# Optimization experiments

Measured on AMD Instinct MI355X. Metric: run time of the kernel, lower is better.

The kernel has to match this reference:

```python
import jax, jax.numpy as jnp
import numpy as np

N_NODES = 100000
N_EDGES = 1600000
F_IN = 128
F_HID = 16


def _gcn_conv(x, src, dst, W, b, n):
    # PyG GCNConv: x' = D^{-1/2} (A + I) D^{-1/2} (x W) + b
    h = x @ W                                   # [N, F_out] transform first (small F)
    deg = jax.ops.segment_sum(jnp.ones_like(dst, dtype=h.dtype), dst, num_segments=n)
    dinv = jnp.where(deg > 0, jax.lax.rsqrt(deg), 0.0)
    norm = dinv[src] * dinv[dst]                # [E+N] edge weights
    msg = h[src] * norm[:, None]                # gather + scale
    out = jax.ops.segment_sum(msg, dst, num_segments=n)  # scatter-add
    return out + b


def setup_inputs() -> dict:
    key = jax.random.key(0)
    k1, k2, k3, k4 = jax.random.split(key, 4)
    x = jax.random.normal(k1, (N_NODES, F_IN), dtype=jnp.float32)
    edge_index = jax.random.randint(k2, (2, N_EDGES), 0, N_NODES, dtype=jnp.int64)
    # Glorot-ish init for the two GCNConv weights
    W1 = jax.random.normal(k3, (F_IN, F_HID), dtype=jnp.float32) * (1.0 / np.sqrt(F_IN))
    b1 = jnp.zeros((F_HID,), dtype=jnp.float32)
    W2 = jax.random.normal(k4, (F_HID, F_IN), dtype=jnp.float32) * (1.0 / np.sqrt(F_HID))
    b2 = jnp.zeros((F_IN,), dtype=jnp.float32)
    return {"x": x, "edge_index": edge_index, "W1": W1, "b1": b1, "W2": W2, "b2": b2}


def reference(x, edge_index, W1, b1, W2, b2):
    n = x.shape[0]
    # add self-loops once (GCNConv default add_self_loops=True)
    loop = jnp.arange(n, dtype=edge_index.dtype)
    src = jnp.concatenate([edge_index[0], loop])
    dst = jnp.concatenate([edge_index[1], loop])
    h = _gcn_conv(x, src, dst, W1, b1, n)
    h = jax.nn.relu(h)
    out = _gcn_conv(h, src, dst, W2, b2, n)
    return out
```

## Files before the change

### kernel.cpp

```cpp
#include <hip/hip_runtime.h>
#include <hip/hip_fp16.h>


#define NN 100000
#define NE 1600000
#define FI 128
#define FH 16
#define CB 64
#define NB 1563
#define GC 512
#define CHUNK 3125
#define SCB 16

__device__ __forceinline__ float fc(const float4& v, int i) {
    return i == 0 ? v.x : i == 1 ? v.y : i == 2 ? v.z : v.w;
}

__global__ __launch_bounds__(256) void k_count(const int* __restrict__ dst,
                                               int* __restrict__ hist) {
    __shared__ int h[NB];
    for (int i = threadIdx.x; i < NB; i += 256) h[i] = 0;
    __syncthreads();
    int base = blockIdx.x * CHUNK;
    for (int i = base + threadIdx.x; i < base + CHUNK; i += 256)
        atomicAdd(&h[dst[i] >> 6], 1);
    __syncthreads();
    for (int b = threadIdx.x; b < NB; b += 256)
        hist[blockIdx.x * NB + b] = h[b];
}

__global__ __launch_bounds__(256) void k_scan_chunks(int* __restrict__ hist,
                                                     int* __restrict__ totals) {
    __shared__ int s[GC * SCB];
    int b0 = blockIdx.x * SCB;
    int o[GC * SCB / 256];
    #pragma unroll
    for (int r = 0; r < GC * SCB / 256; ++r) {
        int idx = r * 256 + threadIdx.x;
        int c = idx >> 4, bl = idx & (SCB - 1), b = b0 + bl;
        int v = (b < NB) ? hist[c * NB + b] : 0;
        s[idx] = v;
        o[r] = v;
    }
    __syncthreads();
    for (int off = 1; off < GC; off <<= 1) {
        int t[GC * SCB / 256];
        #pragma unroll
        for (int r = 0; r < GC * SCB / 256; ++r) {
            int idx = r * 256 + threadIdx.x;
            int c = idx >> 4;
            t[r] = (c >= off) ? s[idx - off * SCB] : 0;
        }
        __syncthreads();
        #pragma unroll
        for (int r = 0; r < GC * SCB / 256; ++r) {
            int idx = r * 256 + threadIdx.x;
            s[idx] += t[r];
        }
        __syncthreads();
    }
    #pragma unroll
    for (int r = 0; r < GC * SCB / 256; ++r) {
        int idx = r * 256 + threadIdx.x;
        int c = idx >> 4, bl = idx & (SCB - 1), b = b0 + bl;
        if (b < NB) {
            hist[c * NB + b] = s[idx] - o[r];
            if (c == GC - 1) totals[b] = s[idx];
        }
    }
}

__global__ __launch_bounds__(1024) void k_scan_buckets(const int* __restrict__ totals,
                                                       int* __restrict__ bucketStart,
                                                       int* __restrict__ rowStart) {
    __shared__ int s[1024];
    int tid = threadIdx.x;
    int i0 = 2 * tid, i1 = i0 + 1;
    int a = (i0 < NB) ? totals[i0] : 0;
    int b = (i1 < NB) ? totals[i1] : 0;
    s[tid] = a + b;
    __syncthreads();
    #pragma unroll
    for (int off = 1; off < 1024; off <<= 1) {
        int t = (tid >= off) ? s[tid - off] : 0;
        __syncthreads();
        s[tid] += t;
        __syncthreads();
    }
    int excl = s[tid] - (a + b);
    if (i0 < NB) bucketStart[i0] = excl;
    if (i1 < NB) bucketStart[i1] = excl + a;
    if (tid == 0) { bucketStart[NB] = NE; rowStart[NN] = NE; }
}

__global__ __launch_bounds__(256) void k_scatter(const int* __restrict__ src,
                                                 const int* __restrict__ dst,
                                                 const int* __restrict__ hist,
                                                 const int* __restrict__ bucketStart,
                                                 int* __restrict__ packed) {
    __shared__ int cur[NB];
    for (int b = threadIdx.x; b < NB; b += 256)
        cur[b] = hist[blockIdx.x * NB + b] + bucketStart[b];
    __syncthreads();
    int base = blockIdx.x * CHUNK;
    for (int i = base + threadIdx.x; i < base + CHUNK; i += 256) {
        int d = dst[i];
        int pos = atomicAdd(&cur[d >> 6], 1);
        packed[pos] = src[i] | ((d & 63) << 17);
    }
}

__global__ __launch_bounds__(256) void k_bsort(const int* __restrict__ packed,
                                               const int* __restrict__ bucketStart,
                                               int* __restrict__ csr,
                                               int* __restrict__ rowStart,
                                               float* __restrict__ dinv) {
    __shared__ int cnt[CB];
    __shared__ int rs[CB];
    __shared__ int cur[CB];
    if (threadIdx.x < CB) cnt[threadIdx.x] = 0;
    __syncthreads();
    int s0 = bucketStart[blockIdx.x], s1 = bucketStart[blockIdx.x + 1];
    for (int i = s0 + threadIdx.x; i < s1; i += 256)
        atomicAdd(&cnt[(packed[i] >> 17) & 63], 1);
    __syncthreads();
    if (threadIdx.x < CB) rs[threadIdx.x] = cnt[threadIdx.x];
    __syncthreads();
    #pragma unroll
    for (int off = 1; off < CB; off <<= 1) {
        int t = 0;
        if (threadIdx.x < CB && threadIdx.x >= off) t = rs[threadIdx.x - off];
        __syncthreads();
        if (threadIdx.x < CB) rs[threadIdx.x] += t;
        __syncthreads();
    }
    if (threadIdx.x < CB) {
        int start = s0 + rs[threadIdx.x] - cnt[threadIdx.x];
        cur[threadIdx.x] = start;
        int node = blockIdx.x * CB + threadIdx.x;
        if (node < NN) {
            rowStart[node] = start;
            dinv[node] = rsqrtf((float)(cnt[threadIdx.x] + 1));
        }
    }
    __syncthreads();
    for (int i = s0 + threadIdx.x; i < s1; i += 256) {
        int pk = packed[i];
        int pos = atomicAdd(&cur[(pk >> 17) & 63], 1);
        csr[pos] = pk & 131071;
    }
}

__global__ __launch_bounds__(256) void k_gemm1(const float* __restrict__ x,
                                               const float* __restrict__ W1,
                                               const float* __restrict__ dinv,
                                               __half2* __restrict__ g1) {
    __shared__ __align__(16) float w[FI * FH];
    float4* w4s = (float4*)w;
    w4s[threadIdx.x] = ((const float4*)W1)[threadIdx.x];
    w4s[threadIdx.x + 256] = ((const float4*)W1)[threadIdx.x + 256];
    __syncthreads();
    int fg = threadIdx.x & 3;
    int ng = threadIdx.x >> 2;
    int r0 = blockIdx.x * 256 + ng * 4;
    const float4* x4 = (const float4*)x;
    int rr[4]; bool val[4];
    #pragma unroll
    for (int i = 0; i < 4; ++i) {
        val[i] = (r0 + i < NN);
        rr[i] = val[i] ? r0 + i : NN - 1;
    }
    float acc[4][4];
    #pragma unroll
    for (int i = 0; i < 4; ++i)
        #pragma unroll
        for (int j = 0; j < 4; ++j) acc[i][j] = 0.f;
    #pragma unroll 2
    for (int k4 = 0; k4 < 32; ++k4) {
        float4 xv[4];
        #pragma unroll
        for (int i = 0; i < 4; ++i) xv[i] = x4[rr[i] * 32 + k4];
        #pragma unroll
        for (int kk = 0; kk < 4; ++kk) {
            float4 wv = w4s[(k4 * 4 + kk) * 4 + fg];
            #pragma unroll
            for (int i = 0; i < 4; ++i) {
                float xk = fc(xv[i], kk);
                acc[i][0] += xk * wv.x; acc[i][1] += xk * wv.y;
                acc[i][2] += xk * wv.z; acc[i][3] += xk * wv.w;
            }
        }
    }
    #pragma unroll
    for (int i = 0; i < 4; ++i) if (val[i]) {
        float dv = dinv[rr[i]];
        g1[rr[i] * 8 + fg * 2]     = __floats2half2_rn(acc[i][0] * dv, acc[i][1] * dv);
        g1[rr[i] * 8 + fg * 2 + 1] = __floats2half2_rn(acc[i][2] * dv, acc[i][3] * dv);
    }
}

template<bool RELU>
__global__ __launch_bounds__(256) void k_agg(const int* __restrict__ csr,
                                             const int* __restrict__ rowStart,
                                             const __half2* __restrict__ gin,
                                             const float* __restrict__ dinv,
                                             const float* __restrict__ b1,
                                             __half2* __restrict__ gh_out,
                                             float2* __restrict__ p2f) {
    int gid = blockIdx.x * 256 + threadIdx.x;
    int node = gid >> 3, c = gid & 7;
    if (node >= NN) return;
    int s0 = rowStart[node], s1 = rowStart[node + 1];
    float2 acc = __half22float2(gin[node * 8 + c]);
    int e = s0;
    for (; e + 3 < s1; e += 4) {
        int i0 = csr[e], i1 = csr[e + 1], i2 = csr[e + 2], i3 = csr[e + 3];
        float2 f0 = __half22float2(gin[i0 * 8 + c]);
        float2 f1 = __half22float2(gin[i1 * 8 + c]);
        float2 f2 = __half22float2(gin[i2 * 8 + c]);
        float2 f3 = __half22float2(gin[i3 * 8 + c]);
        acc.x += (f0.x + f1.x) + (f2.x + f3.x);
        acc.y += (f0.y + f1.y) + (f2.y + f3.y);
    }
    for (; e < s1; ++e) {
        float2 f = __half22float2(gin[csr[e] * 8 + c]);
        acc.x += f.x; acc.y += f.y;
    }
    float dv = dinv[node];
    if (RELU) {
        float2 bb = *(const float2*)(b1 + 2 * c);
        float vx = fmaxf(dv * acc.x + bb.x, 0.f) * dv;
        float vy = fmaxf(dv * acc.y + bb.y, 0.f) * dv;
        gh_out[node * 8 + c] = __floats2half2_rn(vx, vy);
    } else {
        p2f[node * 8 + c] = make_float2(dv * acc.x, dv * acc.y);
    }
}

__global__ __launch_bounds__(256) void k_gemm2(const float* __restrict__ p2s,
                                               const float* __restrict__ W2,
                                               const float* __restrict__ b2,
                                               float* __restrict__ out) {
    __shared__ __align__(16) float w[FH * FI];
    __shared__ __align__(16) float pst[FH][32];
    float4* w4s = (float4*)w;
    w4s[threadIdx.x] = ((const float4*)W2)[threadIdx.x];
    w4s[threadIdx.x + 256] = ((const float4*)W2)[threadIdx.x + 256];
    int base = blockIdx.x * 32;
    {
        int n = threadIdx.x >> 4, k = threadIdx.x & 15;
        int gn = base + n;
        pst[k][n] = (gn < NN) ? p2s[gn * 16 + k] : 0.f;
        n += 16; gn = base + n;
        pst[k][n] = (gn < NN) ? p2s[gn * 16 + k] : 0.f;
    }
    __syncthreads();
    int fg = threadIdx.x & 31;
    int ng = threadIdx.x >> 5;
    float4 bb = ((const float4*)b2)[fg];
    float acc[4][4];
    #pragma unroll
    for (int i = 0; i < 4; ++i) {
        acc[i][0] = bb.x; acc[i][1] = bb.y; acc[i][2] = bb.z; acc[i][3] = bb.w;
    }
    #pragma unroll
    for (int k = 0; k < FH; ++k) {
        float4 xk = *(float4*)&pst[k][ng * 4];
        float4 wv = w4s[k * 32 + fg];
        #pragma unroll
        for (int i = 0; i < 4; ++i) {
            float xv = fc(xk, i);
            acc[i][0] += xv * wv.x; acc[i][1] += xv * wv.y;
            acc[i][2] += xv * wv.z; acc[i][3] += xv * wv.w;
        }
    }
    #pragma unroll
    for (int i = 0; i < 4; ++i) {
        int gn = base + ng * 4 + i;
        if (gn < NN)
            ((float4*)out)[gn * 32 + fg] =
                make_float4(acc[i][0], acc[i][1], acc[i][2], acc[i][3]);
    }
}

extern "C" void kernel_launch(void* const* d_in, const int* in_sizes, int n_in,
                              void* d_out, int out_size, void* d_ws, size_t ws_size,
                              hipStream_t stream) {
    const float* x  = (const float*)d_in[0];
    const int*   ei = (const int*)d_in[1];
    const float* W1 = (const float*)d_in[2];
    const float* b1 = (const float*)d_in[3];
    const float* W2 = (const float*)d_in[4];
    const float* b2 = (const float*)d_in[5];
    float* out = (float*)d_out;

    const int* src = ei;
    const int* dst = ei + NE;

    int*   totals      = (int*)d_ws;
    int*   bucketStart = totals + NB;
    int*   rowStart    = bucketStart + NB + 1;
    float* dinv        = (float*)(rowStart + NN + 1);
    int*   csr         = (int*)(dinv + NN);
    int*   hist        = csr;
    int*   packed      = csr + NE;
    __half2* g1        = (__half2*)packed;
    __half2* g2        = g1 + NN * 8;
    float2*  p2f       = (float2*)(packed + NE);

    k_count       <<<GC, 256, 0, stream>>>(dst, hist);
    k_scan_chunks <<<(NB + SCB - 1) / SCB, 256, 0, stream>>>(hist, totals);
    k_scan_buckets<<<1, 1024, 0, stream>>>(totals, bucketStart, rowStart);
    k_scatter     <<<GC, 256, 0, stream>>>(src, dst, hist, bucketStart, packed);
    k_bsort       <<<NB, 256, 0, stream>>>(packed, bucketStart, csr, rowStart, dinv);

    k_gemm1       <<<(NN + 255) / 256, 256, 0, stream>>>(x, W1, dinv, g1);
    k_agg<true>   <<<(NN * 8) / 256, 256, 0, stream>>>(csr, rowStart, g1, dinv, b1, g2, (float2*)nullptr);
    k_agg<false>  <<<(NN * 8) / 256, 256, 0, stream>>>(csr, rowStart, g2, dinv, b1, (__half2*)nullptr, p2f);
    k_gemm2       <<<(NN + 31) / 32, 256, 0, stream>>>((const float*)p2f, W2, b2, out);
}
```

Before: 227.3 us.

## Fuse gemm1 into count kernel and second aggregation into gemm2

The first GEMM no longer depends on dinv. It runs as extra blocks of the histogram kernel, so the dense transform overlaps with CSR construction. The first aggregation now applies dinv[src] per edge, which adds a random gather per edge. The second aggregation is fused with the W2 GEMM through shared memory, dropping the p2f intermediate round trip and one launch. The g1 buffer moves after the packed region to avoid aliasing with data still live during the sort.

```diff
diff --git a/kernel.cpp b/kernel.cpp
--- a/kernel.cpp
+++ b/kernel.cpp
@@ -16,17 +16,64 @@
     return i == 0 ? v.x : i == 1 ? v.y : i == 2 ? v.z : v.w;
 }
 
-__global__ __launch_bounds__(256) void k_count(const int* __restrict__ dst,
-                                               int* __restrict__ hist) {
+__global__ __launch_bounds__(256) void k_count_gemm1(const int* __restrict__ dst,
+                                                     int* __restrict__ hist,
+                                                     const float* __restrict__ x,
+                                                     const float* __restrict__ W1,
+                                                     __half2* __restrict__ g1) {
     __shared__ int h[NB];
-    for (int i = threadIdx.x; i < NB; i += 256) h[i] = 0;
-    __syncthreads();
-    int base = blockIdx.x * CHUNK;
-    for (int i = base + threadIdx.x; i < base + CHUNK; i += 256)
-        atomicAdd(&h[dst[i] >> 6], 1);
-    __syncthreads();
-    for (int b = threadIdx.x; b < NB; b += 256)
-        hist[blockIdx.x * NB + b] = h[b];
+    __shared__ __align__(16) float w[FI * FH];
+    if (blockIdx.x < GC) {
+        for (int i = threadIdx.x; i < NB; i += 256) h[i] = 0;
+        __syncthreads();
+        int base = blockIdx.x * CHUNK;
+        for (int i = base + threadIdx.x; i < base + CHUNK; i += 256)
+            atomicAdd(&h[dst[i] >> 6], 1);
+        __syncthreads();
+        for (int b = threadIdx.x; b < NB; b += 256)
+            hist[blockIdx.x * NB + b] = h[b];
+    } else {
+        float4* w4s = (float4*)w;
+        w4s[threadIdx.x] = ((const float4*)W1)[threadIdx.x];
+        w4s[threadIdx.x + 256] = ((const float4*)W1)[threadIdx.x + 256];
+        __syncthreads();
+        int fg = threadIdx.x & 3;
+        int ng = threadIdx.x >> 2;
+        int r0 = (blockIdx.x - GC) * 256 + ng * 4;
+        const float4* x4 = (const float4*)x;
+        int rr[4]; bool val[4];
+        #pragma unroll
+        for (int i = 0; i < 4; ++i) {
+            val[i] = (r0 + i < NN);
+            rr[i] = val[i] ? r0 + i : NN - 1;
+        }
+        float acc[4][4];
+        #pragma unroll
+        for (int i = 0; i < 4; ++i)
+            #pragma unroll
+            for (int j = 0; j < 4; ++j) acc[i][j] = 0.f;
+        #pragma unroll 2
+        for (int k4 = 0; k4 < 32; ++k4) {
+            float4 xv[4];
+            #pragma unroll
+            for (int i = 0; i < 4; ++i) xv[i] = x4[rr[i] * 32 + k4];
+            #pragma unroll
+            for (int kk = 0; kk < 4; ++kk) {
+                float4 wv = w4s[(k4 * 4 + kk) * 4 + fg];
+                #pragma unroll
+                for (int i = 0; i < 4; ++i) {
+                    float xk = fc(xv[i], kk);
+                    acc[i][0] += xk * wv.x; acc[i][1] += xk * wv.y;
+                    acc[i][2] += xk * wv.z; acc[i][3] += xk * wv.w;
+                }
+            }
+        }
+        #pragma unroll
+        for (int i = 0; i < 4; ++i) if (val[i]) {
+            g1[rr[i] * 8 + fg * 2]     = __floats2half2_rn(acc[i][0], acc[i][1]);
+            g1[rr[i] * 8 + fg * 2 + 1] = __floats2half2_rn(acc[i][2], acc[i][3]);
+        }
+    }
 }
 
 __global__ __launch_bounds__(256) void k_scan_chunks(int* __restrict__ hist,
@@ -151,117 +198,89 @@
     }
 }
 
-__global__ __launch_bounds__(256) void k_gemm1(const float* __restrict__ x,
-                                               const float* __restrict__ W1,
-                                               const float* __restrict__ dinv,
-                                               __half2* __restrict__ g1) {
-    __shared__ __align__(16) float w[FI * FH];
-    float4* w4s = (float4*)w;
-    w4s[threadIdx.x] = ((const float4*)W1)[threadIdx.x];
-    w4s[threadIdx.x + 256] = ((const float4*)W1)[threadIdx.x + 256];
-    __syncthreads();
-    int fg = threadIdx.x & 3;
-    int ng = threadIdx.x >> 2;
-    int r0 = blockIdx.x * 256 + ng * 4;
-    const float4* x4 = (const float4*)x;
-    int rr[4]; bool val[4];
-    #pragma unroll
-    for (int i = 0; i < 4; ++i) {
-        val[i] = (r0 + i < NN);
-        rr[i] = val[i] ? r0 + i : NN - 1;
-    }
-    float acc[4][4];
-    #pragma unroll
-    for (int i = 0; i < 4; ++i)
-        #pragma unroll
-        for (int j = 0; j < 4; ++j) acc[i][j] = 0.f;
-    #pragma unroll 2
-    for (int k4 = 0; k4 < 32; ++k4) {
-        float4 xv[4];
-        #pragma unroll
-        for (int i = 0; i < 4; ++i) xv[i] = x4[rr[i] * 32 + k4];
-        #pragma unroll
-        for (int kk = 0; kk < 4; ++kk) {
-            float4 wv = w4s[(k4 * 4 + kk) * 4 + fg];
-            #pragma unroll
-            for (int i = 0; i < 4; ++i) {
-                float xk = fc(xv[i], kk);
-                acc[i][0] += xk * wv.x; acc[i][1] += xk * wv.y;
-                acc[i][2] += xk * wv.z; acc[i][3] += xk * wv.w;
-            }
-        }
-    }
-    #pragma unroll
-    for (int i = 0; i < 4; ++i) if (val[i]) {
-        float dv = dinv[rr[i]];
-        g1[rr[i] * 8 + fg * 2]     = __floats2half2_rn(acc[i][0] * dv, acc[i][1] * dv);
-        g1[rr[i] * 8 + fg * 2 + 1] = __floats2half2_rn(acc[i][2] * dv, acc[i][3] * dv);
-    }
-}
-
-template<bool RELU>
-__global__ __launch_bounds__(256) void k_agg(const int* __restrict__ csr,
-                                             const int* __restrict__ rowStart,
-                                             const __half2* __restrict__ gin,
-                                             const float* __restrict__ dinv,
-                                             const float* __restrict__ b1,
-                                             __half2* __restrict__ gh_out,
-                                             float2* __restrict__ p2f) {
+__global__ __launch_bounds__(256) void k_agg1(const int* __restrict__ csr,
+                                              const int* __restrict__ rowStart,
+                                              const __half2* __restrict__ g1,
+                                              const float* __restrict__ dinv,
+                                              const float* __restrict__ b1,
+                                              __half2* __restrict__ g2) {
     int gid = blockIdx.x * 256 + threadIdx.x;
     int node = gid >> 3, c = gid & 7;
     if (node >= NN) return;
     int s0 = rowStart[node], s1 = rowStart[node + 1];
-    float2 acc = __half22float2(gin[node * 8 + c]);
+    float dv = dinv[node];
+    float2 fs = __half22float2(g1[node * 8 + c]);
+    float2 acc = make_float2(dv * fs.x, dv * fs.y);
     int e = s0;
     for (; e + 3 < s1; e += 4) {
         int i0 = csr[e], i1 = csr[e + 1], i2 = csr[e + 2], i3 = csr[e + 3];
-        float2 f0 = __half22float2(gin[i0 * 8 + c]);
-        float2 f1 = __half22float2(gin[i1 * 8 + c]);
-        float2 f2 = __half22float2(gin[i2 * 8 + c]);
-        float2 f3 = __half22float2(gin[i3 * 8 + c]);
-        acc.x += (f0.x + f1.x) + (f2.x + f3.x);
-        acc.y += (f0.y + f1.y) + (f2.y + f3.y);
+        float d0 = dinv[i0], d1 = dinv[i1], d2 = dinv[i2], d3 = dinv[i3];
+        float2 f0 = __half22float2(g1[i0 * 8 + c]);
+        float2 f1 = __half22float2(g1[i1 * 8 + c]);
+        float2 f2 = __half22float2(g1[i2 * 8 + c]);
+        float2 f3 = __half22float2(g1[i3 * 8 + c]);
+        acc.x = fmaf(d0, f0.x, fmaf(d1, f1.x, fmaf(d2, f2.x, fmaf(d3, f3.x, acc.x))));
+        acc.y = fmaf(d0, f0.y, fmaf(d1, f1.y, fmaf(d2, f2.y, fmaf(d3, f3.y, acc.y))));
     }
     for (; e < s1; ++e) {
-        float2 f = __half22float2(gin[csr[e] * 8 + c]);
-        acc.x += f.x; acc.y += f.y;
-    }
-    float dv = dinv[node];
-    if (RELU) {
-        float2 bb = *(const float2*)(b1 + 2 * c);
-        float vx = fmaxf(dv * acc.x + bb.x, 0.f) * dv;
-        float vy = fmaxf(dv * acc.y + bb.y, 0.f) * dv;
-        gh_out[node * 8 + c] = __floats2half2_rn(vx, vy);
-    } else {
-        p2f[node * 8 + c] = make_float2(dv * acc.x, dv * acc.y);
-    }
-}
-
-__global__ __launch_bounds__(256) void k_gemm2(const float* __restrict__ p2s,
-                                               const float* __restrict__ W2,
-                                               const float* __restrict__ b2,
-                                               float* __restrict__ out) {
+        int i0 = csr[e];
+        float d0 = dinv[i0];
+        float2 f = __half22float2(g1[i0 * 8 + c]);
+        acc.x = fmaf(d0, f.x, acc.x);
+        acc.y = fmaf(d0, f.y, acc.y);
+    }
+    float2 bb = *(const float2*)(b1 + 2 * c);
+    float vx = fmaxf(dv * acc.x + bb.x, 0.f) * dv;
+    float vy = fmaxf(dv * acc.y + bb.y, 0.f) * dv;
+    g2[node * 8 + c] = __floats2half2_rn(vx, vy);
+}
+
+__global__ __launch_bounds__(256) void k_aggemm2(const int* __restrict__ csr,
+                                                 const int* __restrict__ rowStart,
+                                                 const float* __restrict__ dinv,
+                                                 const __half2* __restrict__ g2,
+                                                 const float* __restrict__ W2,
+                                                 const float* __restrict__ b2,
+                                                 float* __restrict__ out) {
     __shared__ __align__(16) float w[FH * FI];
     __shared__ __align__(16) float pst[FH][32];
     float4* w4s = (float4*)w;
     w4s[threadIdx.x] = ((const float4*)W2)[threadIdx.x];
     w4s[threadIdx.x + 256] = ((const float4*)W2)[threadIdx.x + 256];
     int base = blockIdx.x * 32;
-    {
-        int n = threadIdx.x >> 4, k = threadIdx.x & 15;
-        int gn = base + n;
-        pst[k][n] = (gn < NN) ? p2s[gn * 16 + k] : 0.f;
-        n += 16; gn = base + n;
-        pst[k][n] = (gn < NN) ? p2s[gn * 16 + k] : 0.f;
-    }
+    int ln = threadIdx.x >> 3, c = threadIdx.x & 7;
+    int node = base + ln;
+    float2 acc = make_float2(0.f, 0.f);
+    if (node < NN) {
+        int s0 = rowStart[node], s1 = rowStart[node + 1];
+        acc = __half22float2(g2[node * 8 + c]);
+        int e = s0;
+        for (; e + 3 < s1; e += 4) {
+            int i0 = csr[e], i1 = csr[e + 1], i2 = csr[e + 2], i3 = csr[e + 3];
+            float2 f0 = __half22float2(g2[i0 * 8 + c]);
+            float2 f1 = __half22float2(g2[i1 * 8 + c]);
+            float2 f2 = __half22float2(g2[i2 * 8 + c]);
+            float2 f3 = __half22float2(g2[i3 * 8 + c]);
+            acc.x += (f0.x + f1.x) + (f2.x + f3.x);
+            acc.y += (f0.y + f1.y) + (f2.y + f3.y);
+        }
+        for (; e < s1; ++e) {
+            float2 f = __half22float2(g2[csr[e] * 8 + c]);
+            acc.x += f.x; acc.y += f.y;
+        }
+        float dv = dinv[node];
+        acc.x *= dv; acc.y *= dv;
+    }
+    pst[2 * c][ln]     = acc.x;
+    pst[2 * c + 1][ln] = acc.y;
     __syncthreads();
     int fg = threadIdx.x & 31;
     int ng = threadIdx.x >> 5;
     float4 bb = ((const float4*)b2)[fg];
-    float acc[4][4];
+    float a2[4][4];
     #pragma unroll
     for (int i = 0; i < 4; ++i) {
-        acc[i][0] = bb.x; acc[i][1] = bb.y; acc[i][2] = bb.z; acc[i][3] = bb.w;
+        a2[i][0] = bb.x; a2[i][1] = bb.y; a2[i][2] = bb.z; a2[i][3] = bb.w;
     }
     #pragma unroll
     for (int k = 0; k < FH; ++k) {
@@ -270,8 +289,8 @@
         #pragma unroll
         for (int i = 0; i < 4; ++i) {
             float xv = fc(xk, i);
-            acc[i][0] += xv * wv.x; acc[i][1] += xv * wv.y;
-            acc[i][2] += xv * wv.z; acc[i][3] += xv * wv.w;
+            a2[i][0] += xv * wv.x; a2[i][1] += xv * wv.y;
+            a2[i][2] += xv * wv.z; a2[i][3] += xv * wv.w;
         }
     }
     #pragma unroll
@@ -279,7 +298,7 @@
         int gn = base + ng * 4 + i;
         if (gn < NN)
             ((float4*)out)[gn * 32 + fg] =
-                make_float4(acc[i][0], acc[i][1], acc[i][2], acc[i][3]);
+                make_float4(a2[i][0], a2[i][1], a2[i][2], a2[i][3]);
     }
 }
 
@@ -304,18 +323,14 @@
     int*   csr         = (int*)(dinv + NN);
     int*   hist        = csr;
     int*   packed      = csr + NE;
-    __half2* g1        = (__half2*)packed;
+    __half2* g1        = (__half2*)(packed + NE);
     __half2* g2        = g1 + NN * 8;
-    float2*  p2f       = (float2*)(packed + NE);
-
-    k_count       <<<GC, 256, 0, stream>>>(dst, hist);
+
+    k_count_gemm1 <<<GC + (NN + 255) / 256, 256, 0, stream>>>(dst, hist, x, W1, g1);
     k_scan_chunks <<<(NB + SCB - 1) / SCB, 256, 0, stream>>>(hist, totals);
     k_scan_buckets<<<1, 1024, 0, stream>>>(totals, bucketStart, rowStart);
     k_scatter     <<<GC, 256, 0, stream>>>(src, dst, hist, bucketStart, packed);
     k_bsort       <<<NB, 256, 0, stream>>>(packed, bucketStart, csr, rowStart, dinv);
-
-    k_gemm1       <<<(NN + 255) / 256, 256, 0, stream>>>(x, W1, dinv, g1);
-    k_agg<true>   <<<(NN * 8) / 256, 256, 0, stream>>>(csr, rowStart, g1, dinv, b1, g2, (float2*)nullptr);
-    k_agg<false>  <<<(NN * 8) / 256, 256, 0, stream>>>(csr, rowStart, g2, dinv, b1, (__half2*)nullptr, p2f);
-    k_gemm2       <<<(NN + 31) / 32, 256, 0, stream>>>((const float*)p2f, W2, b2, out);
-}
+    k_agg1        <<<(NN * 8) / 256, 256, 0, stream>>>(csr, rowStart, g1, dinv, b1, g2);
+    k_aggemm2     <<<(NN + 31) / 32, 256, 0, stream>>>(csr, rowStart, dinv, g2, W2, b2, out);
+}
```

New measurement: 247.1 us. 1.09x slower.
